# Kernel optimization log

Hardware: AMD Instinct MI355X
Metric: run time of the kernel (lower is better)

The kernel has to match this reference:

```python
import jax, jax.numpy as jnp
import numpy as np

CUTOFF = 4          # lattice cutoff radius (module init arg)
NMAX = 64           # padded max neighbors per mobile site (~58 actual at cutoff=4)
BATCH = 131072      # number of independent configurations
B_SOFT = 0.01       # softening constant b in vint
FAR = 1e6           # padding position, masked out


def _rot(c):
    return np.array([[np.cos(c), -np.sin(c)], [np.sin(c), np.cos(c)]])


def _build_geometry():
    """Replicates PotEnergy1P.__init__ (with the intended, bug-fixed math)."""
    s3 = np.sqrt(3.0)
    base = [np.array([0.5, s3 / 6]), np.array([1.0, -s3 / 3]),
            np.array([1.5, s3 / 6]), np.array([1.0, 2 * s3 / 3])]
    mobile = base \
        + [_rot(2 * np.pi / 3) @ p for p in base] \
        + [_rot(4 * np.pi / 3) @ p for p in base]
    mobile = np.stack(mobile)                      # [12, 2]

    def ntopos(n1, n2):
        return np.array([0.5, s3 / 6]) + n1 * np.array([1.0, 0.0]) \
            + n2 * np.array([-0.5, s3 / 2])

    rng = range(-4 * CUTOFF, 4 * CUTOFF)
    grid = np.array([ntopos(n1, n2) for n1 in rng for n2 in rng])  # [G, 2]
    dist = np.linalg.norm(grid[:, None, :] - mobile[None, :, :], axis=-1)  # [G, 12]
    not_mobile = ~np.any(np.isclose(dist, 0.0, atol=1e-8), axis=1)        # [G]

    neighbors = np.full((12, NMAX, 2), FAR, dtype=np.float32)
    mask = np.zeros((12, NMAX), dtype=np.float32)
    for i in range(12):
        idx = np.where(not_mobile & (dist[:, i] < CUTOFF))[0]
        k = len(idx)
        assert k <= NMAX
        neighbors[i, :k] = grid[idx]
        mask[i, :k] = 1.0
    return neighbors, mask


def setup_inputs() -> dict:
    key = jax.random.key(0)
    x = jax.random.normal(key, (BATCH, 24), dtype=jnp.float32)
    neighbors, mask = _build_geometry()
    return {"x": x,
            "neighbors": jnp.asarray(neighbors),
            "mask": jnp.asarray(mask)}


def reference(x, neighbors, mask):
    # x: [B, 24] -> [B, 12, 2] mobile positions
    xr = x.reshape(x.shape[0], -1, 2)
    # pairwise displacement to all padded neighbors: [B, 12, NMAX, 2]
    d = xr[:, :, None, :] - neighbors[None, :, :, :]
    r = jnp.sqrt(jnp.sum(d * d, axis=-1))          # [B, 12, NMAX]
    v = jnp.exp(-r) / (r + B_SOFT)                 # vint with a=1.0, b=0.01
    return jnp.sum(v * mask[None], axis=(1, 2))    # [B] total potential energy
```

## Files before the change

### kernel.cpp

```cpp
#include <hip/hip_runtime.h>

#define NMAX   64
#define NSITES 12
#define SPLIT  4
#define BLOCK  256
#define RS     68

#define B_SOFT 0.01f
#define PAD_C  4.0e4f
#define R2_MAX 248.0f
#define TBL_LO 1392
#define TBL_N  768

__device__ __forceinline__ float f_exact(float r2) {
    const float r = sqrtf(r2);
    return expf(-r) / (r + B_SOFT);
}

__global__ __launch_bounds__(BLOCK, 8)
void pot_energy_kernel(const float* __restrict__ x,
                       const float* __restrict__ neighbors,
                       const float* __restrict__ mask,
                       float* __restrict__ out, int B) {
    __shared__ float  nbx[NSITES][RS];
    __shared__ float  nby[NSITES][RS];
    __shared__ float2 tbl[TBL_N];
    __shared__ int    cnt[NSITES];

    const int tid  = threadIdx.x;
    const int wv   = tid >> 6;
    const int lane = tid & 63;

    for (int i = tid; i < TBL_N; i += BLOCK) {
        const unsigned ii = (unsigned)(i + TBL_LO);
        const float b0 = __builtin_bit_cast(float, ii << 19);
        const float b1 = __builtin_bit_cast(float, (ii + 1u) << 19);
        const float f0 = f_exact(b0);
        const float f1 = f_exact(b1);
        const float fm = f_exact(0.5f * (b0 + b1));
        const float s  = (f1 - f0) / (b1 - b0);
        const float c  = f0 - s * b0 - 0.5f * (0.5f * (f0 + f1) - fm);
        tbl[i] = make_float2(c, s);
    }

    for (int idx = tid; idx < NSITES * RS; idx += BLOCK) {
        const int s = idx / RS, j = idx - s * RS;
        nbx[s][j] = PAD_C;
        nby[s][j] = PAD_C;
    }
    __syncthreads();

    for (int s = wv; s < NSITES; s += 4) {
        const bool keep = mask[s * NMAX + lane] > 0.5f;
        const unsigned long long bal = __ballot(keep);
        if (keep) {
            const int pos = __popcll(bal & ((1ull << lane) - 1ull));
            const float2 p = ((const float2*)neighbors)[s * NMAX + lane];
            nbx[s][pos] = p.x;
            nby[s][pos] = p.y;
        }
        if (lane == 0) cnt[s] = __popcll(bal);
    }
    __syncthreads();

    int m = 0;
    #pragma unroll
    for (int s = 0; s < NSITES; ++s) m = max(m, cnt[s]);
    m = (__builtin_amdgcn_readfirstlane(m) + 3) & ~3;

    const int gtid = blockIdx.x * BLOCK + tid;
    const int e = gtid >> 2;
    const int q = gtid & 3;
    if (e >= B) return;

    const float2* xp = (const float2*)(x + (size_t)gtid * 6);
    const float2 p0 = xp[0], p1 = xp[1], p2 = xp[2];
    const float xs_[3] = { p0.x, p1.x, p2.x };
    const float ys_[3] = { p0.y, p1.y, p2.y };

    float accC = 0.f, accS = 0.f;
    #pragma unroll
    for (int s = 0; s < 3; ++s) {
        const int site = q * 3 + s;
        const float xs = xs_[s];
        const float ys = ys_[s];
        const float* __restrict__ rx = nbx[site];
        const float* __restrict__ ry = nby[site];
        #pragma unroll 2
        for (int j0 = 0; j0 < m; j0 += 4) {
            const float4 nx4 = *(const float4*)(rx + j0);
            const float4 ny4 = *(const float4*)(ry + j0);
            const float nx[4] = { nx4.x, nx4.y, nx4.z, nx4.w };
            const float ny[4] = { ny4.x, ny4.y, ny4.z, ny4.w };
            #pragma unroll
            for (int k = 0; k < 4; ++k) {
                const float dx = xs - nx[k];
                const float dy = ys - ny[k];
                float r2 = fmaf(dy, dy, dx * dx);
                r2 = fminf(r2, R2_MAX);
                const unsigned bits = __builtin_bit_cast(unsigned, r2);
                int idx = (int)(bits >> 19) - TBL_LO;
                idx = idx < 0 ? 0 : idx;
                const float2 cs = tbl[idx];
                accC += cs.x;
                accS = fmaf(cs.y, r2, accS);
            }
        }
    }

    float acc = accC + accS;
    acc += __shfl_xor(acc, 1);
    acc += __shfl_xor(acc, 2);
    if (q == 0) out[e] = acc;
}

extern "C" void kernel_launch(void* const* d_in, const int* in_sizes, int n_in,
                              void* d_out, int out_size, void* d_ws, size_t ws_size,
                              hipStream_t stream) {
    const float* x   = (const float*)d_in[0];
    const float* nbr = (const float*)d_in[1];
    const float* msk = (const float*)d_in[2];
    float* out = (float*)d_out;

    const int B = in_sizes[0] / 24;
    const int total_threads = B * SPLIT;
    const int blocks = (total_threads + BLOCK - 1) / BLOCK;
    pot_energy_kernel<<<blocks, BLOCK, 0, stream>>>(x, nbr, msk, out, B);
}
```

Before: 82.97 us.

## Precompute neighbor tables in a one-block init kernel and streamline lookup indexing

Moves the per-block table construction (exp/sqrt/div per entry) and neighbor compaction into a single-block init kernel that writes to a global workspace. The main kernel then copies the prepared data into shared memory with float4 loads. It also computes the table address directly from the float bits via fmed3 clamping and packed v2f arithmetic. In exchange there is an extra kernel launch with a serial dependency, and each block still does a global-to-shared copy, while the lookup changes the byte layout so the table sits at an offset inside a larger shared buffer.

```diff
diff --git a/kernel.cpp b/kernel.cpp
--- a/kernel.cpp
+++ b/kernel.cpp
@@ -1,4 +1,5 @@
 #include <hip/hip_runtime.h>
+#include <math.h>
 
 #define NMAX   64
 #define NSITES 12
@@ -12,24 +13,51 @@
 #define TBL_LO 1392
 #define TBL_N  768
 
+#define NB_FLOATS  (NSITES * RS)
+#define TBL_OFF    (TBL_LO * 8)
+#define SMEM_BYTES (TBL_OFF + TBL_N * 8)
+
+#define WS_TBL_F   1664
+#define WS_FLOATS  3200
+__device__ __align__(16) float g_ws[WS_FLOATS];
+__device__ int g_m;
+
+typedef float v2f __attribute__((ext_vector_type(2)));
+typedef float v4f __attribute__((ext_vector_type(4)));
+
 __device__ __forceinline__ float f_exact(float r2) {
     const float r = sqrtf(r2);
     return expf(-r) / (r + B_SOFT);
 }
 
-__global__ __launch_bounds__(BLOCK, 8)
-void pot_energy_kernel(const float* __restrict__ x,
-                       const float* __restrict__ neighbors,
-                       const float* __restrict__ mask,
-                       float* __restrict__ out, int B) {
-    __shared__ float  nbx[NSITES][RS];
-    __shared__ float  nby[NSITES][RS];
-    __shared__ float2 tbl[TBL_N];
-    __shared__ int    cnt[NSITES];
-
+__global__ void init_kernel(const float* __restrict__ neighbors,
+                            const float* __restrict__ mask) {
+    __shared__ int cnt[NSITES];
     const int tid  = threadIdx.x;
     const int wv   = tid >> 6;
     const int lane = tid & 63;
+
+    for (int i = tid; i < 2 * NB_FLOATS; i += BLOCK) g_ws[i] = PAD_C;
+    __syncthreads();
+
+    for (int s = wv; s < NSITES; s += 4) {
+        const bool keep = mask[s * NMAX + lane] > 0.5f;
+        const unsigned long long bal = __ballot(keep);
+        if (keep) {
+            const int pos = __popcll(bal & ((1ull << lane) - 1ull));
+            const float2 p = ((const float2*)neighbors)[s * NMAX + lane];
+            g_ws[s * RS + pos]             = p.x;
+            g_ws[NB_FLOATS + s * RS + pos] = p.y;
+        }
+        if (lane == 0) cnt[s] = __popcll(bal);
+    }
+    __syncthreads();
+    if (tid == 0) {
+        int m = 0;
+        #pragma unroll
+        for (int s = 0; s < NSITES; ++s) m = max(m, cnt[s]);
+        g_m = (m + 3) & ~3;
+    }
 
     for (int i = tid; i < TBL_N; i += BLOCK) {
         const unsigned ii = (unsigned)(i + TBL_LO);
@@ -38,35 +66,37 @@
         const float f0 = f_exact(b0);
         const float f1 = f_exact(b1);
         const float fm = f_exact(0.5f * (b0 + b1));
-        const float s  = (f1 - f0) / (b1 - b0);
-        const float c  = f0 - s * b0 - 0.5f * (0.5f * (f0 + f1) - fm);
-        tbl[i] = make_float2(c, s);
+        const float sl = (f1 - f0) / (b1 - b0);
+        const float c  = f0 - sl * b0 - 0.5f * (0.5f * (f0 + f1) - fm);
+        g_ws[WS_TBL_F + 2 * i]     = c;
+        g_ws[WS_TBL_F + 2 * i + 1] = sl;
     }
+}
 
-    for (int idx = tid; idx < NSITES * RS; idx += BLOCK) {
-        const int s = idx / RS, j = idx - s * RS;
-        nbx[s][j] = PAD_C;
-        nby[s][j] = PAD_C;
+__global__ __launch_bounds__(BLOCK, 8)
+void pot_energy_kernel(const float* __restrict__ x,
+                       float* __restrict__ out, int B) {
+    __shared__ __align__(16) char smem[SMEM_BYTES];
+    const int tid = threadIdx.x;
+
+    {
+        const float4* s0 = (const float4*)g_ws;
+        float4* d0 = (float4*)smem;
+        #pragma unroll
+        for (int i = 0; i < 2; ++i) {
+            const int idx = tid + i * BLOCK;
+            if (idx < (2 * NB_FLOATS) / 4) d0[idx] = s0[idx];
+        }
+        const float4* s1 = (const float4*)(g_ws + WS_TBL_F);
+        float4* d1 = (float4*)(smem + TBL_OFF);
+        #pragma unroll
+        for (int i = 0; i < 2; ++i) {
+            const int idx = tid + i * BLOCK;
+            if (idx < (TBL_N * 8) / 16) d1[idx] = s1[idx];
+        }
     }
+    const int m = g_m;
     __syncthreads();
-
-    for (int s = wv; s < NSITES; s += 4) {
-        const bool keep = mask[s * NMAX + lane] > 0.5f;
-        const unsigned long long bal = __ballot(keep);
-        if (keep) {
-            const int pos = __popcll(bal & ((1ull << lane) - 1ull));
-            const float2 p = ((const float2*)neighbors)[s * NMAX + lane];
-            nbx[s][pos] = p.x;
-            nby[s][pos] = p.y;
-        }
-        if (lane == 0) cnt[s] = __popcll(bal);
-    }
-    __syncthreads();
-
-    int m = 0;
-    #pragma unroll
-    for (int s = 0; s < NSITES; ++s) m = max(m, cnt[s]);
-    m = (__builtin_amdgcn_readfirstlane(m) + 3) & ~3;
 
     const int gtid = blockIdx.x * BLOCK + tid;
     const int e = gtid >> 2;
@@ -78,32 +108,35 @@
     const float xs_[3] = { p0.x, p1.x, p2.x };
     const float ys_[3] = { p0.y, p1.y, p2.y };
 
+    const float R2MINF = __builtin_bit_cast(float, 0x2B800000u);
+
     float accC = 0.f, accS = 0.f;
     #pragma unroll
     for (int s = 0; s < 3; ++s) {
         const int site = q * 3 + s;
-        const float xs = xs_[s];
-        const float ys = ys_[s];
-        const float* __restrict__ rx = nbx[site];
-        const float* __restrict__ ry = nby[site];
+        const float* __restrict__ rx = (const float*)smem + site * RS;
+        const float* __restrict__ ry = rx + NB_FLOATS;
+        const v2f xs2 = { xs_[s], xs_[s] };
+        const v2f ys2 = { ys_[s], ys_[s] };
         #pragma unroll 2
         for (int j0 = 0; j0 < m; j0 += 4) {
-            const float4 nx4 = *(const float4*)(rx + j0);
-            const float4 ny4 = *(const float4*)(ry + j0);
-            const float nx[4] = { nx4.x, nx4.y, nx4.z, nx4.w };
-            const float ny[4] = { ny4.x, ny4.y, ny4.z, ny4.w };
+            const v4f nx4 = *(const v4f*)(rx + j0);
+            const v4f ny4 = *(const v4f*)(ry + j0);
+            const v2f dxA = xs2 - nx4.xy;
+            const v2f dxB = xs2 - nx4.zw;
+            const v2f dyA = ys2 - ny4.xy;
+            const v2f dyB = ys2 - ny4.zw;
+            const v2f r2A = __builtin_elementwise_fma(dyA, dyA, dxA * dxA);
+            const v2f r2B = __builtin_elementwise_fma(dyB, dyB, dxB * dxB);
+            const float r2k[4] = { r2A.x, r2A.y, r2B.x, r2B.y };
             #pragma unroll
             for (int k = 0; k < 4; ++k) {
-                const float dx = xs - nx[k];
-                const float dy = ys - ny[k];
-                float r2 = fmaf(dy, dy, dx * dx);
-                r2 = fminf(r2, R2_MAX);
-                const unsigned bits = __builtin_bit_cast(unsigned, r2);
-                int idx = (int)(bits >> 19) - TBL_LO;
-                idx = idx < 0 ? 0 : idx;
-                const float2 cs = tbl[idx];
+                const float r2c = __builtin_amdgcn_fmed3f(r2k[k], R2MINF, R2_MAX);
+                const unsigned off =
+                    (__builtin_bit_cast(unsigned, r2c) >> 16) & 0xFFF8u;
+                const float2 cs = *(const float2*)(smem + off);
                 accC += cs.x;
-                accS = fmaf(cs.y, r2, accS);
+                accS = fmaf(cs.y, r2c, accS);
             }
         }
     }
@@ -123,7 +156,10 @@
     float* out = (float*)d_out;
 
     const int B = in_sizes[0] / 24;
+
+    init_kernel<<<1, BLOCK, 0, stream>>>(nbr, msk);
+
     const int total_threads = B * SPLIT;
     const int blocks = (total_threads + BLOCK - 1) / BLOCK;
-    pot_energy_kernel<<<blocks, BLOCK, 0, stream>>>(x, nbr, msk, out, B);
+    pot_energy_kernel<<<blocks, BLOCK, 0, stream>>>(x, out, B);
 }
```

Measured after the change: 80.95 us. 2.4% less time.

## Precompute finer piecewise-constant lookup table in init kernel, halve threads per config

Applied to the files above, without the earlier changes.

Moves table and neighbor-compaction setup into a separate init kernel that writes to a global workspace, which each block then copies into shared memory. The interpolation table changes from a linear (c,s) table to a finer 6144-entry piecewise-constant midpoint table, removing the FMA and halving LDS bytes per lookup. It also interleaves neighbor x/y storage, uses fmed3 clamping, and processes six sites per thread with two threads per configuration instead of four. Per-block setup cost drops, but a larger shared-memory footprint (~30KB) lowers occupancy. The piecewise-constant approximation also changes the accuracy characteristics.

```diff
diff --git a/kernel.cpp b/kernel.cpp
--- a/kernel.cpp
+++ b/kernel.cpp
@@ -1,116 +1,133 @@
 #include <hip/hip_runtime.h>
+#include <math.h>
 
 #define NMAX   64
 #define NSITES 12
-#define SPLIT  4
+#define SPLIT  2
 #define BLOCK  256
-#define RS     68
 
 #define B_SOFT 0.01f
 #define PAD_C  4.0e4f
 #define R2_MAX 248.0f
-#define TBL_LO 1392
-#define TBL_N  768
+#define R2_MIN_BITS 0x2B800000u
+
+#define TBL_N     6144
+#define TBL_BYTES (TBL_N * 4)
+
+#define NPAIR  66
+#define ROWF   (NPAIR * 2)
+#define NB_F   (NSITES * ROWF)
+#define WS_F   (TBL_N + NB_F)
+#define SMEM_F WS_F
+
+__device__ __align__(16) float g_ws[WS_F];
+__device__ int g_m;
+
+typedef float v4f __attribute__((ext_vector_type(4)));
 
 __device__ __forceinline__ float f_exact(float r2) {
     const float r = sqrtf(r2);
     return expf(-r) / (r + B_SOFT);
 }
 
-__global__ __launch_bounds__(BLOCK, 8)
-void pot_energy_kernel(const float* __restrict__ x,
-                       const float* __restrict__ neighbors,
-                       const float* __restrict__ mask,
-                       float* __restrict__ out, int B) {
-    __shared__ float  nbx[NSITES][RS];
-    __shared__ float  nby[NSITES][RS];
-    __shared__ float2 tbl[TBL_N];
-    __shared__ int    cnt[NSITES];
+#define INIT_BLOCKS 25
 
-    const int tid  = threadIdx.x;
-    const int wv   = tid >> 6;
-    const int lane = tid & 63;
+__global__ void init_kernel(const float* __restrict__ neighbors,
+                            const float* __restrict__ mask) {
+    const int tid = threadIdx.x;
+    const int gid = blockIdx.x * BLOCK + tid;
 
-    for (int i = tid; i < TBL_N; i += BLOCK) {
-        const unsigned ii = (unsigned)(i + TBL_LO);
-        const float b0 = __builtin_bit_cast(float, ii << 19);
-        const float b1 = __builtin_bit_cast(float, (ii + 1u) << 19);
-        const float f0 = f_exact(b0);
-        const float f1 = f_exact(b1);
-        const float fm = f_exact(0.5f * (b0 + b1));
-        const float s  = (f1 - f0) / (b1 - b0);
-        const float c  = f0 - s * b0 - 0.5f * (0.5f * (f0 + f1) - fm);
-        tbl[i] = make_float2(c, s);
+    if (gid < TBL_N) {
+        const unsigned b0 = R2_MIN_BITS + ((unsigned)gid << 16);
+        const unsigned b1 = b0 + (1u << 16);
+        const float f0 = f_exact(__builtin_bit_cast(float, b0));
+        const float f1 = f_exact(__builtin_bit_cast(float, b1));
+        g_ws[gid] = 0.5f * (f0 + f1);
     }
 
-    for (int idx = tid; idx < NSITES * RS; idx += BLOCK) {
-        const int s = idx / RS, j = idx - s * RS;
-        nbx[s][j] = PAD_C;
-        nby[s][j] = PAD_C;
+    if (blockIdx.x == 0) {
+        __shared__ int cnt[NSITES];
+        for (int i = tid; i < NB_F; i += BLOCK) g_ws[TBL_N + i] = PAD_C;
+        __syncthreads();
+
+        const int wv = tid >> 6, lane = tid & 63;
+        for (int s = wv; s < NSITES; s += 4) {
+            const bool keep = mask[s * NMAX + lane] > 0.5f;
+            const unsigned long long bal = __ballot(keep);
+            if (keep) {
+                const int pos = __popcll(bal & ((1ull << lane) - 1ull));
+                const float2 p = ((const float2*)neighbors)[s * NMAX + lane];
+                g_ws[TBL_N + s * ROWF + 2 * pos]     = p.x;
+                g_ws[TBL_N + s * ROWF + 2 * pos + 1] = p.y;
+            }
+            if (lane == 0) cnt[s] = __popcll(bal);
+        }
+        __syncthreads();
+        if (tid == 0) {
+            int m = 0;
+            #pragma unroll
+            for (int s = 0; s < NSITES; ++s) m = max(m, cnt[s]);
+            g_m = (m + 3) & ~3;
+        }
     }
+}
+
+__global__ __launch_bounds__(BLOCK, 4)
+void pot_energy_kernel(const float* __restrict__ x,
+                       float* __restrict__ out, int B) {
+    __shared__ __align__(16) float smem[SMEM_F];
+    const int tid = threadIdx.x;
+
+    {
+        const float4* s4 = (const float4*)g_ws;
+        float4* d4 = (float4*)smem;
+        for (int i = tid; i < WS_F / 4; i += BLOCK) d4[i] = s4[i];
+    }
+    const int m = g_m;
     __syncthreads();
 
-    for (int s = wv; s < NSITES; s += 4) {
-        const bool keep = mask[s * NMAX + lane] > 0.5f;
-        const unsigned long long bal = __ballot(keep);
-        if (keep) {
-            const int pos = __popcll(bal & ((1ull << lane) - 1ull));
-            const float2 p = ((const float2*)neighbors)[s * NMAX + lane];
-            nbx[s][pos] = p.x;
-            nby[s][pos] = p.y;
-        }
-        if (lane == 0) cnt[s] = __popcll(bal);
-    }
-    __syncthreads();
-
-    int m = 0;
-    #pragma unroll
-    for (int s = 0; s < NSITES; ++s) m = max(m, cnt[s]);
-    m = (__builtin_amdgcn_readfirstlane(m) + 3) & ~3;
-
     const int gtid = blockIdx.x * BLOCK + tid;
-    const int e = gtid >> 2;
-    const int q = gtid & 3;
+    const int e = gtid >> 1;
+    const int q = gtid & 1;
     if (e >= B) return;
 
-    const float2* xp = (const float2*)(x + (size_t)gtid * 6);
-    const float2 p0 = xp[0], p1 = xp[1], p2 = xp[2];
-    const float xs_[3] = { p0.x, p1.x, p2.x };
-    const float ys_[3] = { p0.y, p1.y, p2.y };
+    const float4* xp = (const float4*)(x + (size_t)e * 24 + q * 12);
+    const float4 x0 = xp[0], x1 = xp[1], x2 = xp[2];
+    const float xs_[6] = { x0.x, x0.z, x1.x, x1.z, x2.x, x2.z };
+    const float ys_[6] = { x0.y, x0.w, x1.y, x1.w, x2.y, x2.w };
 
-    float accC = 0.f, accS = 0.f;
+    const float R2MINF = __builtin_bit_cast(float, R2_MIN_BITS);
+
+    float acc0 = 0.f, acc1 = 0.f;
     #pragma unroll
-    for (int s = 0; s < 3; ++s) {
-        const int site = q * 3 + s;
+    for (int s = 0; s < 6; ++s) {
+        const int site = q * 6 + s;
         const float xs = xs_[s];
         const float ys = ys_[s];
-        const float* __restrict__ rx = nbx[site];
-        const float* __restrict__ ry = nby[site];
+        const float* __restrict__ row = smem + TBL_N + site * ROWF;
         #pragma unroll 2
         for (int j0 = 0; j0 < m; j0 += 4) {
-            const float4 nx4 = *(const float4*)(rx + j0);
-            const float4 ny4 = *(const float4*)(ry + j0);
-            const float nx[4] = { nx4.x, nx4.y, nx4.z, nx4.w };
-            const float ny[4] = { ny4.x, ny4.y, ny4.z, ny4.w };
+            const v4f a = *(const v4f*)(row + 2 * j0);
+            const v4f b = *(const v4f*)(row + 2 * j0 + 4);
+            const float nx[4] = { a.x, a.z, b.x, b.z };
+            const float ny[4] = { a.y, a.w, b.y, b.w };
             #pragma unroll
             for (int k = 0; k < 4; ++k) {
                 const float dx = xs - nx[k];
                 const float dy = ys - ny[k];
                 float r2 = fmaf(dy, dy, dx * dx);
-                r2 = fminf(r2, R2_MAX);
-                const unsigned bits = __builtin_bit_cast(unsigned, r2);
-                int idx = (int)(bits >> 19) - TBL_LO;
-                idx = idx < 0 ? 0 : idx;
-                const float2 cs = tbl[idx];
-                accC += cs.x;
-                accS = fmaf(cs.y, r2, accS);
+                r2 = __builtin_amdgcn_fmed3f(r2, R2MINF, R2_MAX);
+                const unsigned t =
+                    __builtin_bit_cast(unsigned, r2) - R2_MIN_BITS;
+                const unsigned off = (t >> 14) & 0xFFFFFFFCu;
+                const float c = *(const float*)((const char*)smem + off);
+                if (k & 1) acc1 += c; else acc0 += c;
             }
         }
     }
 
-    float acc = accC + accS;
+    float acc = acc0 + acc1;
     acc += __shfl_xor(acc, 1);
-    acc += __shfl_xor(acc, 2);
     if (q == 0) out[e] = acc;
 }
 
@@ -123,7 +140,10 @@
     float* out = (float*)d_out;
 
     const int B = in_sizes[0] / 24;
+
+    init_kernel<<<INIT_BLOCKS, BLOCK, 0, stream>>>(nbr, msk);
+
     const int total_threads = B * SPLIT;
     const int blocks = (total_threads + BLOCK - 1) / BLOCK;
-    pot_energy_kernel<<<blocks, BLOCK, 0, stream>>>(x, nbr, msk, out, B);
+    pot_energy_kernel<<<blocks, BLOCK, 0, stream>>>(x, out, B);
 }
```

Measured after the change: 85.92 us. 3.6% more time.
